# Kernel optimization log

Measured on AMD Instinct MI355X. Metric: run time of the kernel, lower is better.

## Reference

```python
import math
import jax, jax.numpy as jnp
import numpy as np

NUM_LEVELS = 3
K = 9          # filter_size
SIGMA = 2.0
OMEGA_X = 0.25
OMEGA_Y = 0.25
C = 64         # channels


def _fan_filter():
    # low-pass Gaussian, shape (C,1,K,K)
    ax = jnp.arange(K, dtype=jnp.float32) - (K - 1) / 2.0
    xx, yy = jnp.meshgrid(ax, ax, indexing='ij')
    lp = jnp.exp(-(xx ** 2 + yy ** 2) / (2.0 * SIGMA ** 2))
    lp = lp / jnp.sum(lp)
    lp = jnp.tile(lp[None, None], (C, 1, 1, 1))
    # high-pass: negate and add delta at center of channel 0 ONLY (faithful to source)
    hp = -lp
    c = K // 2
    hp = hp.at[0, 0, c, c].add(1.0)
    # fan modulation
    cy = jnp.arange(K, dtype=jnp.float32) - K // 2
    cx = jnp.arange(K, dtype=jnp.float32) - K // 2
    y, x = jnp.meshgrid(cy, cx, indexing='ij')
    mod = jnp.cos(2.0 * math.pi * (OMEGA_X * x + OMEGA_Y * y))
    return hp * mod


def _shear_sample(x, s):
    """affine_grid(theta=[[1,s,0],[0,1,0]]) + grid_sample(bilinear, zeros, align_corners=False)."""
    B, Cc, H, W = x.shape
    dt = x.dtype
    # align_corners=False normalized base grid
    xn = (2.0 * jnp.arange(W, dtype=dt) + 1.0) / W - 1.0  # (W,)
    yn = (2.0 * jnp.arange(H, dtype=dt) + 1.0) / H - 1.0  # (H,)
    gx = xn[None, :] + s * yn[:, None]                    # (H,W)
    gy = jnp.broadcast_to(yn[:, None], (H, W))            # (H,W)
    # unnormalize (align_corners=False)
    ix = ((gx + 1.0) * W - 1.0) / 2.0
    iy = ((gy + 1.0) * H - 1.0) / 2.0
    ix0 = jnp.floor(ix); iy0 = jnp.floor(iy)
    ix1 = ix0 + 1.0;     iy1 = iy0 + 1.0
    wx1 = ix - ix0; wx0 = 1.0 - wx1
    wy1 = iy - iy0; wy0 = 1.0 - wy1

    def gather(yi, xi):
        yc = jnp.clip(yi, 0, H - 1).astype(jnp.int32)
        xc = jnp.clip(xi, 0, W - 1).astype(jnp.int32)
        valid = ((yi >= 0) & (yi < H) & (xi >= 0) & (xi < W)).astype(dt)
        return x[:, :, yc, xc] * valid  # (B,C,H,W)

    out = (gather(iy0, ix0) * (wy0 * wx0)
           + gather(iy0, ix1) * (wy0 * wx1)
           + gather(iy1, ix0) * (wy1 * wx0)
           + gather(iy1, ix1) * (wy1 * wx1))
    return out


def _dwconv(x, filt):
    # depthwise cross-correlation, padding K//2 (matches F.conv2d groups=C)
    return jax.lax.conv_general_dilated(
        x, filt, window_strides=(1, 1),
        padding=[(K // 2, K // 2), (K // 2, K // 2)],
        dimension_numbers=('NCHW', 'OIHW', 'NCHW'),
        feature_group_count=C)


def _dfb(x, filt):
    out1 = _dwconv(_shear_sample(x, 1.0), filt)
    out2 = _dwconv(_shear_sample(x, -1.0), filt)
    return out1, out2


def _binary_dfb(x, filt, level):
    if level == 0:
        return [x]
    d1, d2 = _dfb(x, filt)
    return _binary_dfb(d1, filt, level - 1) + _binary_dfb(d2, filt, level - 1)


def setup_inputs() -> dict:
    key = jax.random.key(0)
    x = jax.random.normal(key, (4, C, 256, 256), dtype=jnp.float32)
    filt = _fan_filter()  # buffer (C,1,K,K)
    return {"x": x, "filt": filt}


def reference(x, filt):
    # stack of 2^NUM_LEVELS directional subbands, shape (8, B, C, H, W)
    return jnp.stack(_binary_dfb(x, filt, NUM_LEVELS))
```

## Files before the change

### kernel.cpp

```cpp
#include <hip/hip_runtime.h>
#include <hip/hip_fp16.h>


#define B_ 4
#define C_ 64
#define H_ 256
#define W_ 256
#define TH 32
#define SROWS (TH + 8)
#define SCOLS (W_ + 8)
#define NPB 2048
#define PSTRIDE 260
#define PPLANE (H_ * PSTRIDE)

struct alignas(4) h8 { unsigned int u[4]; };

template<bool SRC_H, bool DST_H>
__global__ __launch_bounds__(256) void shear_sepconv_kernel(
    const void* __restrict__ in_, void* __restrict__ dst_,
    const float* __restrict__ filt, int parity)
{
    __shared__ float s_sh[SROWS][SCOLS];

    const int tid  = threadIdx.x;
    const int bid  = (int)blockIdx.x;
    const int tile = bid & 7;
    const int c    = (bid >> 3) & 63;
    const int b    = bid >> 9;
    const int h0   = tile * TH;
    const int sign = parity ? -1 : 1;
    const int off  = parity ? 127 : -128;

    const int plane_idx = b * C_ + c;

    {
        const int wave = tid >> 6;
        const int lane = tid & 63;

        if (tid < 80) {
            const int r = tid >> 1;
            *(float4*)&s_sh[r][(tid & 1) ? 260 : 0] = make_float4(0.f, 0.f, 0.f, 0.f);
        }

        #pragma unroll
        for (int u = 0; u < 10; ++u) {
            const int r  = wave + u * 4;
            const int hr = h0 + r - 4;
            float4 v = make_float4(0.f, 0.f, 0.f, 0.f);
            if ((unsigned)hr < 256u) {
                if (SRC_H) {
                    const __half* rowh = (const __half*)in_
                        + (size_t)plane_idx * PPLANE + (size_t)hr * PSTRIDE;
                    const int d  = off + sign * hr + 4 + lane * 4;
                    const int m  = d & ~1;
                    const int mc = min(max(m, 0), 258);
                    const bool qhi   = (d & 1) != 0;
                    const bool valid = (unsigned)d < 260u;
                    union { h8 raw; __half2 h2[4]; } U;
                    U.raw = *(const h8*)(rowh + mc);
                    const float2 g01 = __half22float2(U.h2[0]);
                    const float2 g23 = __half22float2(U.h2[1]);
                    const float2 g45 = __half22float2(U.h2[2]);
                    const float t0 = qhi ? g01.y : g01.x;
                    const float t1 = qhi ? g23.x : g01.y;
                    const float t2 = qhi ? g23.y : g23.x;
                    const float t3 = qhi ? g45.x : g23.y;
                    const float t4 = qhi ? g45.y : g45.x;
                    v.x = valid ? 0.5f * (t0 + t1) : 0.f;
                    v.y = valid ? 0.5f * (t1 + t2) : 0.f;
                    v.z = valid ? 0.5f * (t2 + t3) : 0.f;
                    v.w = valid ? 0.5f * (t3 + t4) : 0.f;
                } else {
                    const float* row = (const float*)in_
                        + (size_t)plane_idx * (H_ * W_) + (size_t)hr * W_;
                    const int c0 = off + sign * hr + lane * 4;
                    const int i0 = min(max(c0,     0), 255);
                    const int i1 = min(max(c0 + 1, 0), 255);
                    const int i2 = min(max(c0 + 2, 0), 255);
                    const int i3 = min(max(c0 + 3, 0), 255);
                    const int i4 = min(max(c0 + 4, 0), 255);
                    float t0 = row[i0];
                    float t1 = row[i1];
                    float t2 = row[i2];
                    float t3 = row[i3];
                    float t4 = row[i4];
                    t0 = ((unsigned)c0       < 256u) ? t0 : 0.f;
                    t1 = ((unsigned)(c0 + 1) < 256u) ? t1 : 0.f;
                    t2 = ((unsigned)(c0 + 2) < 256u) ? t2 : 0.f;
                    t3 = ((unsigned)(c0 + 3) < 256u) ? t3 : 0.f;
                    t4 = ((unsigned)(c0 + 4) < 256u) ? t4 : 0.f;
                    v.x = 0.5f * (t0 + t1);
                    v.y = 0.5f * (t1 + t2);
                    v.z = 0.5f * (t2 + t3);
                    v.w = 0.5f * (t3 + t4);
                }
            }
            *(float4*)&s_sh[r][4 + lane * 4] = v;
        }
    }

    const float* f1 = filt + 81;
    const float A4  = sqrtf(fmaxf(-f1[4 * 9 + 4], 0.f));
    const float rA4 = 1.f / A4;
    const float A0  = -f1[0 * 9 + 4] * rA4;
    const float A2  = -f1[2 * 9 + 4] * rA4;
    const float A6  = -f1[6 * 9 + 4] * rA4;
    const float A8  = -f1[8 * 9 + 4] * rA4;
    const float B5  = sqrtf(fmaxf(f1[5 * 9 + 5], 0.f));
    const float rB5 = 1.f / B5;
    const float B1  = f1[1 * 9 + 5] * rB5;
    const float B3  = f1[3 * 9 + 5] * rB5;
    const float B7  = f1[7 * 9 + 5] * rB5;
    const float vc[9] = {-A0, B1, -A2, B3, -A4, B5, -A6, B7, -A8};

    __syncthreads();

    const int rg   = tid >> 6;
    const int lane = tid & 63;
    const int w0   = lane * 4;

    float acc[8][4];
    #pragma unroll
    for (int i = 0; i < 8; ++i)
        #pragma unroll
        for (int j = 0; j < 4; ++j) acc[i][j] = 0.f;

    __builtin_amdgcn_s_setprio(1);
    #pragma unroll
    for (int t = 0; t < 16; ++t) {
        const int rr = rg * 8 + t;
        const float4 sa  = *(const float4*)&s_sh[rr][w0];
        const float4 sb  = *(const float4*)&s_sh[rr][w0 + 4];
        const float4 sc4 = *(const float4*)&s_sh[rr][w0 + 8];
        const float s[12] = {sa.x, sa.y, sa.z, sa.w,
                             sb.x, sb.y, sb.z, sb.w,
                             sc4.x, sc4.y, sc4.z, sc4.w};
        float ha[4], hb[4];
        #pragma unroll
        for (int j = 0; j < 4; ++j) {
            ha[j] = fmaf(A8, s[j + 8],
                    fmaf(A6, s[j + 6],
                    fmaf(A4, s[j + 4],
                    fmaf(A2, s[j + 2], A0 * s[j]))));
            hb[j] = fmaf(B7, s[j + 7],
                    fmaf(B5, s[j + 5],
                    fmaf(B3, s[j + 3], B1 * s[j + 1])));
        }
        #pragma unroll
        for (int i = 0; i < 8; ++i) {
            const int ky = t - i;
            if (ky >= 0 && ky < 9) {
                #pragma unroll
                for (int j = 0; j < 4; ++j) {
                    const float hv = (ky & 1) ? hb[j] : ha[j];
                    acc[i][j] = fmaf(vc[ky], hv, acc[i][j]);
                }
            }
        }
    }
    __builtin_amdgcn_s_setprio(0);

    if (c == 0) {
        #pragma unroll
        for (int i = 0; i < 8; ++i) {
            const float4 sv = *(const float4*)&s_sh[rg * 8 + i + 4][w0 + 4];
            acc[i][0] += sv.x; acc[i][1] += sv.y; acc[i][2] += sv.z; acc[i][3] += sv.w;
        }
    }

    if (DST_H) {
        __half* plane = (__half*)dst_ + (size_t)plane_idx * PPLANE;
        if (lane < 8) {
            uint2 z; z.x = 0u; z.y = 0u;
            *(uint2*)(plane + (size_t)(h0 + rg * 8 + lane + 1) * PSTRIDE) = z;
        }
        if (bid == 0 && tid == 8) {
            uint2 z; z.x = 0u; z.y = 0u;
            *(uint2*)dst_ = z;
        }
        __half* optr = plane + (size_t)(h0 + rg * 8) * PSTRIDE + 4 + w0;
        #pragma unroll
        for (int i = 0; i < 8; ++i) {
            union { __half2 h2; unsigned int u; } p0, p1;
            p0.h2 = __floats2half2_rn(acc[i][0], acc[i][1]);
            p1.h2 = __floats2half2_rn(acc[i][2], acc[i][3]);
            uint2 pk; pk.x = p0.u; pk.y = p1.u;
            *(uint2*)(optr + (size_t)i * PSTRIDE) = pk;
        }
    } else {
        float* optr = (float*)dst_
            + (((size_t)plane_idx) * H_ + h0 + rg * 8) * (size_t)W_ + w0;
        #pragma unroll
        for (int i = 0; i < 8; ++i) {
            const float4 v = {acc[i][0], acc[i][1], acc[i][2], acc[i][3]};
            *(float4*)(optr + (size_t)i * W_) = v;
        }
    }
}

extern "C" void kernel_launch(void* const* d_in, const int* in_sizes, int n_in,
                              void* d_out, int out_size, void* d_ws, size_t ws_size,
                              hipStream_t stream) {
    const float* x    = (const float*)d_in[0];
    const float* filt = (const float*)d_in[1];
    float* out = (float*)d_out;
    void*  wsb = d_ws;
    const size_t N = (size_t)B_ * C_ * H_ * W_;

    float* S[8];
    for (int k = 0; k < 8; ++k) S[k] = out + (size_t)k * N;

    void* Bh  = (void*)S[0];
    void* BAh = (void*)S[2];
    void* BBh = (void*)S[3];
    void* Ah  = (void*)S[1];
    void* AAh = (void*)S[2];
    void* ABh = wsb;

    const dim3 grid(NPB);
    const dim3 block(256);

    #define L(SH, DH, src, dst, par) \
        shear_sepconv_kernel<SH, DH><<<grid, block, 0, stream>>>(src, dst, filt, par)

    L(false, true , x,   Bh,   1);
    L(true , true , Bh,  BAh,  0);
    L(true , false, BAh, S[4], 0);
    L(true , false, BAh, S[5], 1);
    L(true , true , Bh,  BBh,  1);
    L(true , false, BBh, S[6], 0);
    L(true , false, BBh, S[7], 1);
    L(false, true , x,   Ah,   0);
    L(true , true , Ah,  AAh,  0);
    L(true , true , Ah,  ABh,  1);
    L(true , false, AAh, S[0], 0);
    L(true , false, AAh, S[1], 1);
    L(true , false, ABh, S[2], 0);
    L(true , false, ABh, S[3], 1);
    #undef L
}
```

Before: 394.0 us.

## Process two row tiles per block, prefetching the second tile into registers

Half-precision-source launches now use a pipelined kernel where each block handles two 32-row tiles, halving the grid. Before computing the first tile it issues global loads for the second tile's rows into registers, so that memory traffic overlaps the first tile's compute. The fp32-source first-level kernel keeps the old one-tile-per-block structure. In exchange, register pressure rises from holding ten h8 vectors across the compute, and fewer blocks are available to hide latency.

Result: faster. 385.7 us (-2.1%).

```diff
diff --git a/kernel.cpp b/kernel.cpp
--- a/kernel.cpp
+++ b/kernel.cpp
@@ -10,111 +10,59 @@
 #define SROWS (TH + 8)
 #define SCOLS (W_ + 8)
 #define NPB 2048
+#define NPB2 1024
 #define PSTRIDE 260
 #define PPLANE (H_ * PSTRIDE)
 
 struct alignas(4) h8 { unsigned int u[4]; };
 
-template<bool SRC_H, bool DST_H>
-__global__ __launch_bounds__(256) void shear_sepconv_kernel(
-    const void* __restrict__ in_, void* __restrict__ dst_,
-    const float* __restrict__ filt, int parity)
-{
-    __shared__ float s_sh[SROWS][SCOLS];
-
+struct Factors { float A0, A2, A4, A6, A8, B1, B3, B5, B7, vc[9]; };
+
+static __device__ __forceinline__ Factors mk_factors(const float* __restrict__ filt)
+{
+    const float* f1 = filt + 81;
+    Factors F;
+    F.A4 = sqrtf(fmaxf(-f1[4 * 9 + 4], 0.f));
+    const float rA4 = 1.f / F.A4;
+    F.A0 = -f1[0 * 9 + 4] * rA4;  F.A2 = -f1[2 * 9 + 4] * rA4;
+    F.A6 = -f1[6 * 9 + 4] * rA4;  F.A8 = -f1[8 * 9 + 4] * rA4;
+    F.B5 = sqrtf(fmaxf(f1[5 * 9 + 5], 0.f));
+    const float rB5 = 1.f / F.B5;
+    F.B1 = f1[1 * 9 + 5] * rB5;  F.B3 = f1[3 * 9 + 5] * rB5;
+    F.B7 = f1[7 * 9 + 5] * rB5;
+    F.vc[0] = -F.A0; F.vc[1] = F.B1; F.vc[2] = -F.A2; F.vc[3] = F.B3;
+    F.vc[4] = -F.A4; F.vc[5] = F.B5; F.vc[6] = -F.A6; F.vc[7] = F.B7;
+    F.vc[8] = -F.A8;
+    return F;
+}
+
+static __device__ __forceinline__ float4 shear_avg_h(const h8 raw, int d)
+{
+    union { h8 r; __half2 h2[4]; } U; U.r = raw;
+    const bool qhi   = (d & 1) != 0;
+    const bool valid = (unsigned)d < 260u;
+    const float2 g01 = __half22float2(U.h2[0]);
+    const float2 g23 = __half22float2(U.h2[1]);
+    const float2 g45 = __half22float2(U.h2[2]);
+    const float t0 = qhi ? g01.y : g01.x;
+    const float t1 = qhi ? g23.x : g01.y;
+    const float t2 = qhi ? g23.y : g23.x;
+    const float t3 = qhi ? g45.x : g23.y;
+    const float t4 = qhi ? g45.y : g45.x;
+    float4 v;
+    v.x = valid ? 0.5f * (t0 + t1) : 0.f;
+    v.y = valid ? 0.5f * (t1 + t2) : 0.f;
+    v.z = valid ? 0.5f * (t2 + t3) : 0.f;
+    v.w = valid ? 0.5f * (t3 + t4) : 0.f;
+    return v;
+}
+
+template<bool DST_H>
+static __device__ __forceinline__ void compute_store(
+    float (&s_sh)[SROWS][SCOLS], void* __restrict__ dst_, const Factors& F,
+    int plane_idx, int c, int h0t, bool first_pad)
+{
     const int tid  = threadIdx.x;
-    const int bid  = (int)blockIdx.x;
-    const int tile = bid & 7;
-    const int c    = (bid >> 3) & 63;
-    const int b    = bid >> 9;
-    const int h0   = tile * TH;
-    const int sign = parity ? -1 : 1;
-    const int off  = parity ? 127 : -128;
-
-    const int plane_idx = b * C_ + c;
-
-    {
-        const int wave = tid >> 6;
-        const int lane = tid & 63;
-
-        if (tid < 80) {
-            const int r = tid >> 1;
-            *(float4*)&s_sh[r][(tid & 1) ? 260 : 0] = make_float4(0.f, 0.f, 0.f, 0.f);
-        }
-
-        #pragma unroll
-        for (int u = 0; u < 10; ++u) {
-            const int r  = wave + u * 4;
-            const int hr = h0 + r - 4;
-            float4 v = make_float4(0.f, 0.f, 0.f, 0.f);
-            if ((unsigned)hr < 256u) {
-                if (SRC_H) {
-                    const __half* rowh = (const __half*)in_
-                        + (size_t)plane_idx * PPLANE + (size_t)hr * PSTRIDE;
-                    const int d  = off + sign * hr + 4 + lane * 4;
-                    const int m  = d & ~1;
-                    const int mc = min(max(m, 0), 258);
-                    const bool qhi   = (d & 1) != 0;
-                    const bool valid = (unsigned)d < 260u;
-                    union { h8 raw; __half2 h2[4]; } U;
-                    U.raw = *(const h8*)(rowh + mc);
-                    const float2 g01 = __half22float2(U.h2[0]);
-                    const float2 g23 = __half22float2(U.h2[1]);
-                    const float2 g45 = __half22float2(U.h2[2]);
-                    const float t0 = qhi ? g01.y : g01.x;
-                    const float t1 = qhi ? g23.x : g01.y;
-                    const float t2 = qhi ? g23.y : g23.x;
-                    const float t3 = qhi ? g45.x : g23.y;
-                    const float t4 = qhi ? g45.y : g45.x;
-                    v.x = valid ? 0.5f * (t0 + t1) : 0.f;
-                    v.y = valid ? 0.5f * (t1 + t2) : 0.f;
-                    v.z = valid ? 0.5f * (t2 + t3) : 0.f;
-                    v.w = valid ? 0.5f * (t3 + t4) : 0.f;
-                } else {
-                    const float* row = (const float*)in_
-                        + (size_t)plane_idx * (H_ * W_) + (size_t)hr * W_;
-                    const int c0 = off + sign * hr + lane * 4;
-                    const int i0 = min(max(c0,     0), 255);
-                    const int i1 = min(max(c0 + 1, 0), 255);
-                    const int i2 = min(max(c0 + 2, 0), 255);
-                    const int i3 = min(max(c0 + 3, 0), 255);
-                    const int i4 = min(max(c0 + 4, 0), 255);
-                    float t0 = row[i0];
-                    float t1 = row[i1];
-                    float t2 = row[i2];
-                    float t3 = row[i3];
-                    float t4 = row[i4];
-                    t0 = ((unsigned)c0       < 256u) ? t0 : 0.f;
-                    t1 = ((unsigned)(c0 + 1) < 256u) ? t1 : 0.f;
-                    t2 = ((unsigned)(c0 + 2) < 256u) ? t2 : 0.f;
-                    t3 = ((unsigned)(c0 + 3) < 256u) ? t3 : 0.f;
-                    t4 = ((unsigned)(c0 + 4) < 256u) ? t4 : 0.f;
-                    v.x = 0.5f * (t0 + t1);
-                    v.y = 0.5f * (t1 + t2);
-                    v.z = 0.5f * (t2 + t3);
-                    v.w = 0.5f * (t3 + t4);
-                }
-            }
-            *(float4*)&s_sh[r][4 + lane * 4] = v;
-        }
-    }
-
-    const float* f1 = filt + 81;
-    const float A4  = sqrtf(fmaxf(-f1[4 * 9 + 4], 0.f));
-    const float rA4 = 1.f / A4;
-    const float A0  = -f1[0 * 9 + 4] * rA4;
-    const float A2  = -f1[2 * 9 + 4] * rA4;
-    const float A6  = -f1[6 * 9 + 4] * rA4;
-    const float A8  = -f1[8 * 9 + 4] * rA4;
-    const float B5  = sqrtf(fmaxf(f1[5 * 9 + 5], 0.f));
-    const float rB5 = 1.f / B5;
-    const float B1  = f1[1 * 9 + 5] * rB5;
-    const float B3  = f1[3 * 9 + 5] * rB5;
-    const float B7  = f1[7 * 9 + 5] * rB5;
-    const float vc[9] = {-A0, B1, -A2, B3, -A4, B5, -A6, B7, -A8};
-
-    __syncthreads();
-
     const int rg   = tid >> 6;
     const int lane = tid & 63;
     const int w0   = lane * 4;
@@ -138,13 +86,13 @@
         float ha[4], hb[4];
         #pragma unroll
         for (int j = 0; j < 4; ++j) {
-            ha[j] = fmaf(A8, s[j + 8],
-                    fmaf(A6, s[j + 6],
-                    fmaf(A4, s[j + 4],
-                    fmaf(A2, s[j + 2], A0 * s[j]))));
-            hb[j] = fmaf(B7, s[j + 7],
-                    fmaf(B5, s[j + 5],
-                    fmaf(B3, s[j + 3], B1 * s[j + 1])));
+            ha[j] = fmaf(F.A8, s[j + 8],
+                    fmaf(F.A6, s[j + 6],
+                    fmaf(F.A4, s[j + 4],
+                    fmaf(F.A2, s[j + 2], F.A0 * s[j]))));
+            hb[j] = fmaf(F.B7, s[j + 7],
+                    fmaf(F.B5, s[j + 5],
+                    fmaf(F.B3, s[j + 3], F.B1 * s[j + 1])));
         }
         #pragma unroll
         for (int i = 0; i < 8; ++i) {
@@ -153,7 +101,7 @@
                 #pragma unroll
                 for (int j = 0; j < 4; ++j) {
                     const float hv = (ky & 1) ? hb[j] : ha[j];
-                    acc[i][j] = fmaf(vc[ky], hv, acc[i][j]);
+                    acc[i][j] = fmaf(F.vc[ky], hv, acc[i][j]);
                 }
             }
         }
@@ -172,13 +120,13 @@
         __half* plane = (__half*)dst_ + (size_t)plane_idx * PPLANE;
         if (lane < 8) {
             uint2 z; z.x = 0u; z.y = 0u;
-            *(uint2*)(plane + (size_t)(h0 + rg * 8 + lane + 1) * PSTRIDE) = z;
-        }
-        if (bid == 0 && tid == 8) {
+            *(uint2*)(plane + (size_t)(h0t + rg * 8 + lane + 1) * PSTRIDE) = z;
+        }
+        if (first_pad && tid == 8) {
             uint2 z; z.x = 0u; z.y = 0u;
             *(uint2*)dst_ = z;
         }
-        __half* optr = plane + (size_t)(h0 + rg * 8) * PSTRIDE + 4 + w0;
+        __half* optr = plane + (size_t)(h0t + rg * 8) * PSTRIDE + 4 + (lane * 4);
         #pragma unroll
         for (int i = 0; i < 8; ++i) {
             union { __half2 h2; unsigned int u; } p0, p1;
@@ -189,13 +137,145 @@
         }
     } else {
         float* optr = (float*)dst_
-            + (((size_t)plane_idx) * H_ + h0 + rg * 8) * (size_t)W_ + w0;
+            + (((size_t)plane_idx) * H_ + h0t + rg * 8) * (size_t)W_ + w0;
         #pragma unroll
         for (int i = 0; i < 8; ++i) {
             const float4 v = {acc[i][0], acc[i][1], acc[i][2], acc[i][3]};
             *(float4*)(optr + (size_t)i * W_) = v;
         }
     }
+}
+
+template<bool DST_H>
+__global__ __launch_bounds__(256) void shear_pipe_kernel(
+    const void* __restrict__ in_, void* __restrict__ dst_,
+    const float* __restrict__ filt, int parity)
+{
+    __shared__ float s_sh[SROWS][SCOLS];
+
+    const int tid  = threadIdx.x;
+    const int bid  = (int)blockIdx.x;
+    const int pr   = bid & 3;
+    const int c    = (bid >> 2) & 63;
+    const int b    = bid >> 8;
+    const int h0   = pr * 64;
+    const int sign = parity ? -1 : 1;
+    const int off  = parity ? 127 : -128;
+    const int wave = tid >> 6;
+    const int lane = tid & 63;
+    const int plane_idx = b * C_ + c;
+    const __half* src = (const __half*)in_ + (size_t)plane_idx * PPLANE;
+
+    if (tid < 80) {
+        const int r = tid >> 1;
+        *(float4*)&s_sh[r][(tid & 1) ? 260 : 0] = make_float4(0.f, 0.f, 0.f, 0.f);
+    }
+
+    #pragma unroll
+    for (int u = 0; u < 10; ++u) {
+        const int r  = wave + u * 4;
+        const int hr = h0 + r - 4;
+        float4 v = make_float4(0.f, 0.f, 0.f, 0.f);
+        if ((unsigned)hr < 256u) {
+            const __half* rowh = src + (size_t)hr * PSTRIDE;
+            const int d  = off + sign * hr + 4 + lane * 4;
+            const int mc = min(max(d & ~1, 0), 258);
+            const h8 raw = *(const h8*)(rowh + mc);
+            v = shear_avg_h(raw, d);
+        }
+        *(float4*)&s_sh[r][4 + lane * 4] = v;
+    }
+
+    h8 R[10] = {};
+    #pragma unroll
+    for (int u = 0; u < 10; ++u) {
+        const int hr = h0 + 28 + wave + u * 4;
+        if ((unsigned)hr < 256u) {
+            const __half* rowh = src + (size_t)hr * PSTRIDE;
+            const int d  = off + sign * hr + 4 + lane * 4;
+            const int mc = min(max(d & ~1, 0), 258);
+            R[u] = *(const h8*)(rowh + mc);
+        }
+    }
+    __builtin_amdgcn_sched_barrier(0);
+
+    const Factors F = mk_factors(filt);
+
+    __syncthreads();
+    compute_store<DST_H>(s_sh, dst_, F, plane_idx, c, h0, bid == 0);
+    __syncthreads();
+
+    #pragma unroll
+    for (int u = 0; u < 10; ++u) {
+        const int r  = wave + u * 4;
+        const int hr = h0 + 28 + r;
+        float4 v = make_float4(0.f, 0.f, 0.f, 0.f);
+        if ((unsigned)hr < 256u) {
+            const int d = off + sign * hr + 4 + lane * 4;
+            v = shear_avg_h(R[u], d);
+        }
+        *(float4*)&s_sh[r][4 + lane * 4] = v;
+    }
+    __syncthreads();
+    compute_store<DST_H>(s_sh, dst_, F, plane_idx, c, h0 + TH, false);
+}
+
+__global__ __launch_bounds__(256) void shear_x_kernel(
+    const float* __restrict__ in, void* __restrict__ dst_,
+    const float* __restrict__ filt, int parity)
+{
+    __shared__ float s_sh[SROWS][SCOLS];
+
+    const int tid  = threadIdx.x;
+    const int bid  = (int)blockIdx.x;
+    const int tile = bid & 7;
+    const int c    = (bid >> 3) & 63;
+    const int b    = bid >> 9;
+    const int h0   = tile * TH;
+    const int sign = parity ? -1 : 1;
+    const int off  = parity ? 127 : -128;
+    const int plane_idx = b * C_ + c;
+
+    {
+        const int wave = tid >> 6;
+        const int lane = tid & 63;
+
+        if (tid < 80) {
+            const int r = tid >> 1;
+            *(float4*)&s_sh[r][(tid & 1) ? 260 : 0] = make_float4(0.f, 0.f, 0.f, 0.f);
+        }
+
+        #pragma unroll
+        for (int u = 0; u < 10; ++u) {
+            const int r  = wave + u * 4;
+            const int hr = h0 + r - 4;
+            float4 v = make_float4(0.f, 0.f, 0.f, 0.f);
+            if ((unsigned)hr < 256u) {
+                const float* row = in + (size_t)plane_idx * (H_ * W_)
+                                      + (size_t)hr * W_;
+                const int c0 = off + sign * hr + lane * 4;
+                float t0 = row[min(max(c0,     0), 255)];
+                float t1 = row[min(max(c0 + 1, 0), 255)];
+                float t2 = row[min(max(c0 + 2, 0), 255)];
+                float t3 = row[min(max(c0 + 3, 0), 255)];
+                float t4 = row[min(max(c0 + 4, 0), 255)];
+                t0 = ((unsigned)c0       < 256u) ? t0 : 0.f;
+                t1 = ((unsigned)(c0 + 1) < 256u) ? t1 : 0.f;
+                t2 = ((unsigned)(c0 + 2) < 256u) ? t2 : 0.f;
+                t3 = ((unsigned)(c0 + 3) < 256u) ? t3 : 0.f;
+                t4 = ((unsigned)(c0 + 4) < 256u) ? t4 : 0.f;
+                v.x = 0.5f * (t0 + t1);
+                v.y = 0.5f * (t1 + t2);
+                v.z = 0.5f * (t2 + t3);
+                v.w = 0.5f * (t3 + t4);
+            }
+            *(float4*)&s_sh[r][4 + lane * 4] = v;
+        }
+    }
+
+    const Factors F = mk_factors(filt);
+    __syncthreads();
+    compute_store<true>(s_sh, dst_, F, plane_idx, c, h0, bid == 0);
 }
 
 extern "C" void kernel_launch(void* const* d_in, const int* in_sizes, int n_in,
@@ -217,25 +297,29 @@
     void* AAh = (void*)S[2];
     void* ABh = wsb;
 
-    const dim3 grid(NPB);
     const dim3 block(256);
-
-    #define L(SH, DH, src, dst, par) \
-        shear_sepconv_kernel<SH, DH><<<grid, block, 0, stream>>>(src, dst, filt, par)
-
-    L(false, true , x,   Bh,   1);
-    L(true , true , Bh,  BAh,  0);
-    L(true , false, BAh, S[4], 0);
-    L(true , false, BAh, S[5], 1);
-    L(true , true , Bh,  BBh,  1);
-    L(true , false, BBh, S[6], 0);
-    L(true , false, BBh, S[7], 1);
-    L(false, true , x,   Ah,   0);
-    L(true , true , Ah,  AAh,  0);
-    L(true , true , Ah,  ABh,  1);
-    L(true , false, AAh, S[0], 0);
-    L(true , false, AAh, S[1], 1);
-    L(true , false, ABh, S[2], 0);
-    L(true , false, ABh, S[3], 1);
-    #undef L
-}
+    const dim3 gridX(NPB);
+    const dim3 gridP(NPB2);
+
+    #define LX(src, dst, par) \
+        shear_x_kernel<<<gridX, block, 0, stream>>>(src, dst, filt, par)
+    #define LP(DH, src, dst, par) \
+        shear_pipe_kernel<DH><<<gridP, block, 0, stream>>>(src, dst, filt, par)
+
+    LX(x, Bh, 1);
+    LP(true , Bh,  BAh,  0);
+    LP(false, BAh, S[4], 0);
+    LP(false, BAh, S[5], 1);
+    LP(true , Bh,  BBh,  1);
+    LP(false, BBh, S[6], 0);
+    LP(false, BBh, S[7], 1);
+    LX(x, Ah, 0);
+    LP(true , Ah,  AAh,  0);
+    LP(true , Ah,  ABh,  1);
+    LP(false, AAh, S[0], 0);
+    LP(false, AAh, S[1], 1);
+    LP(false, ABh, S[2], 0);
+    LP(false, ABh, S[3], 1);
+    #undef LX
+    #undef LP
+}
```
